# Kernel optimization log

Hardware: AMD Instinct MI355X
Metric: run time of the kernel (lower is better)

## Reference

```python
import jax, jax.numpy as jnp
import numpy as np

# dims (match init_kwargs)
S = 2048      # sequence_length
H = 2048      # hidden_size
NH = 32       # num_attention_heads
KVH = 8       # num_key_value_heads
HD = 64       # head_dim
WIN = 128     # sliding_window
QM = NH // KVH
SM_SCALE = 1.0 / float(np.sqrt(HD))


def _rope_rotate(x, cos, sin):
    # x: [S, n, HD]; cos/sin: [S, HD//2]
    x1, x2 = jnp.split(x, 2, axis=-1)
    c = cos[:, None, :].astype(x.dtype)
    s = sin[:, None, :].astype(x.dtype)
    return jnp.concatenate([x1 * c - x2 * s, x2 * c + x1 * s], axis=-1)


def setup_inputs() -> dict:
    key = jax.random.key(0)
    ks = jax.random.split(key, 6)
    x = jax.random.normal(ks[0], (S, H), jnp.float32)
    qkv_dim = HD * (NH + 2 * KVH)
    qkv_kernel = jax.random.normal(ks[1], (H, qkv_dim), jnp.float32) * 0.02
    qkv_bias = jnp.zeros((qkv_dim,), jnp.float32)
    out_kernel = jax.random.normal(ks[2], (NH * HD, H), jnp.float32) * 0.02
    out_bias = jnp.zeros((H,), jnp.float32)
    sinks = jax.random.normal(ks[3], (NH,), jnp.float32) * 0.02
    # RoPE tables: [S, HD//2]
    pos = np.arange(S, dtype=np.float32)
    inv_freq = 1.0 / (10000.0 ** (np.arange(HD // 2, dtype=np.float32) / (HD // 2)))
    ang = pos[:, None] * inv_freq[None, :]
    cos_table = jnp.asarray(np.cos(ang), jnp.float32)
    sin_table = jnp.asarray(np.sin(ang), jnp.float32)
    # causal + sliding-window additive mask [S, S]
    qi = np.arange(S, dtype=np.int32)[:, None]
    ki = np.arange(S, dtype=np.int32)[None, :]
    m = np.where(ki > qi, -np.inf, 0.0).astype(np.float32)
    m = np.where(ki < qi - WIN, -np.inf, m).astype(np.float32)
    mask = jnp.asarray(m)
    return {"x": x, "qkv_kernel": qkv_kernel, "qkv_bias": qkv_bias,
            "out_kernel": out_kernel, "out_bias": out_bias, "sinks": sinks,
            "cos_table": cos_table, "sin_table": sin_table, "mask": mask}


def reference(x, qkv_kernel, qkv_bias, out_kernel, out_bias, sinks, cos_table, sin_table, mask):
    xf = x.astype(jnp.float32)
    qkv = jnp.dot(xf, qkv_kernel, precision=jax.lax.Precision.HIGHEST) + qkv_bias  # [S, qkv_dim]
    q_end = NH * HD
    k_end = q_end + KVH * HD
    q = qkv[:, :q_end].reshape(S, NH, HD)          # NH = KVH*QM
    k = qkv[:, q_end:k_end].reshape(S, KVH, HD)
    v = qkv[:, k_end:].reshape(S, KVH, HD)
    q = _rope_rotate(q, cos_table, sin_table).reshape(S, KVH, QM, HD)
    k = _rope_rotate(k, cos_table, sin_table)
    # logits: [KVH, QM, S_q, S_k]; K broadcast across q_mult (GQA)
    logits = jnp.einsum('qhmd,khd->hmqk', q, k) * jnp.float32(SM_SCALE)
    logits = logits + mask[None, None, :, :]
    sink = jnp.broadcast_to(sinks.reshape(KVH, QM, 1, 1).astype(jnp.float32), (KVH, QM, S, 1))
    extended = jnp.concatenate([logits, sink], axis=-1)
    weights = jax.nn.softmax(extended, axis=-1)[..., :-1]
    attn = jnp.einsum('hmqk,khd->qhmd', weights, v).reshape(S, NH * HD)
    out = jnp.dot(attn, out_kernel, precision=jax.lax.Precision.HIGHEST) + out_bias
    return out.astype(x.dtype)
```

## Files before the change

### kernel.cpp

```cpp
#include <hip/hip_runtime.h>
#include <hip/hip_bf16.h>
#include <cstdint>

typedef __hip_bfloat16 bf16;
typedef __attribute__((ext_vector_type(8))) __bf16 bf16x8;
typedef __attribute__((ext_vector_type(4))) float f32x4;

static __device__ __forceinline__ void gload_lds16(const void* g, void* l) {
  __builtin_amdgcn_global_load_lds(
      (const __attribute__((address_space(1))) uint32_t*)g,
      (__attribute__((address_space(3))) uint32_t*)l, 16, 0, 0);
}

__global__ void f32_to_bf16_kernel(const float* __restrict__ in, bf16* __restrict__ out, int n4) {
  int i = blockIdx.x * 256 + threadIdx.x;
  if (i >= n4) return;
  const float4 v = reinterpret_cast<const float4*>(in)[i];
  ushort4 o;
  o.x = __builtin_bit_cast(unsigned short, __float2bfloat16(v.x));
  o.y = __builtin_bit_cast(unsigned short, __float2bfloat16(v.y));
  o.z = __builtin_bit_cast(unsigned short, __float2bfloat16(v.z));
  o.w = __builtin_bit_cast(unsigned short, __float2bfloat16(v.w));
  reinterpret_cast<ushort4*>(out)[i] = o;
}

__global__ void transpose_to_bf16_kernel(const float* __restrict__ in, bf16* __restrict__ out,
                                         int R, int C) {
  __shared__ float tile[32][33];
  int c0 = blockIdx.x * 32, r0 = blockIdx.y * 32;
  int tx = threadIdx.x & 31, ty = threadIdx.x >> 5;
#pragma unroll
  for (int i = 0; i < 4; ++i)
    tile[ty + i * 8][tx] = in[(size_t)(r0 + ty + i * 8) * C + c0 + tx];
  __syncthreads();
#pragma unroll
  for (int i = 0; i < 4; ++i)
    out[(size_t)(c0 + ty + i * 8) * R + r0 + tx] = __float2bfloat16(tile[tx][ty + i * 8]);
}

template <int NH, int SSHIFT>
__global__ void rope_kernel(bf16* __restrict__ buf, const float* __restrict__ cosT,
                            const float* __restrict__ sinT) {
  const int idx = blockIdx.x * 256 + threadIdx.x;
  const int c = idx & 3;
  const int h = (idx >> 2) & (NH - 1);
  const int s = idx >> SSHIFT;
  bf16* p = buf + (size_t)s * (NH * 64) + h * 64 + c * 8;
  bf16x8 v1 = *reinterpret_cast<bf16x8*>(p);
  bf16x8 v2 = *reinterpret_cast<bf16x8*>(p + 32);
  const float4 c0 = *reinterpret_cast<const float4*>(&cosT[s * 32 + c * 8]);
  const float4 c1 = *reinterpret_cast<const float4*>(&cosT[s * 32 + c * 8 + 4]);
  const float4 s0 = *reinterpret_cast<const float4*>(&sinT[s * 32 + c * 8]);
  const float4 s1 = *reinterpret_cast<const float4*>(&sinT[s * 32 + c * 8 + 4]);
  const float cs[8] = {c0.x, c0.y, c0.z, c0.w, c1.x, c1.y, c1.z, c1.w};
  const float sn[8] = {s0.x, s0.y, s0.z, s0.w, s1.x, s1.y, s1.z, s1.w};
  bf16x8 o1, o2;
#pragma unroll
  for (int e = 0; e < 8; ++e) {
    const float x1 = (float)v1[e], x2 = (float)v2[e];
    o1[e] = (__bf16)(x1 * cs[e] - x2 * sn[e]);
    o2[e] = (__bf16)(x2 * cs[e] + x1 * sn[e]);
  }
  *reinterpret_cast<bf16x8*>(p) = o1;
  *reinterpret_cast<bf16x8*>(p + 32) = o2;
}

__global__ __launch_bounds__(512, 1)
void gemm1_kernel(const bf16* __restrict__ A, const bf16* __restrict__ Bt,
                  const float* __restrict__ bias,
                  bf16* __restrict__ qb, bf16* __restrict__ kb, bf16* __restrict__ vt) {
  extern __shared__ __align__(16) char smem[];
  constexpr int K = 2048, NK = 32;
  const int lin = blockIdx.x;
  const int wgid = (lin & 7) * 32 + (lin >> 3);
  const int bx = wgid >> 4, by = wgid & 15;
  const int brow = by * 128, bcol = bx * 192;
  const int t = threadIdx.x, lane = t & 63, w = t >> 6;
  const int wr = w >> 2, wc = w & 3;
  const int rr = lane & 15, rg = lane >> 4;

  char* Ab = smem;
  char* Bb = smem + 49152;

  auto stageA = [&](int kt) {
#pragma unroll
    for (int p = 0; p < 2; ++p) {
      const int idx = p * 512 + t;
      const int row = idx >> 3;
      const int cg = (idx & 7) ^ (row & 7);
      gload_lds16(A + (size_t)(brow + row) * K + kt * 64 + cg * 8,
                  Ab + (size_t)(kt % 3) * 16384 + (p * 512 + (t & ~63)) * 16);
    }
  };
  auto stageB = [&](int kt) {
#pragma unroll
    for (int p = 0; p < 3; ++p) {
      const int idx = p * 512 + t;
      const int row = idx >> 3;
      const int cg = (idx & 7) ^ (row & 7);
      gload_lds16(Bt + (size_t)(bcol + row) * K + kt * 64 + cg * 8,
                  Bb + (size_t)(kt % 3) * 24576 + (p * 512 + (t & ~63)) * 16);
    }
  };

  f32x4 acc[4][3];
#pragma unroll
  for (int i = 0; i < 4; ++i)
#pragma unroll
    for (int j = 0; j < 3; ++j) acc[i][j] = f32x4{0.f, 0.f, 0.f, 0.f};

  stageA(0); stageB(0); stageA(1); stageB(1);
  asm volatile("s_waitcnt vmcnt(5)" ::: "memory");
  __builtin_amdgcn_s_barrier();

  for (int kt = 0; kt < NK; ++kt) {
    const char* Ar = Ab + (size_t)(kt % 3) * 16384;
    const char* Br = Bb + (size_t)(kt % 3) * 24576;
#pragma unroll
    for (int ks = 0; ks < 2; ++ks) {
      bf16x8 af[4], bfr[3];
      const int c = ks * 4 + rg;
#pragma unroll
      for (int i = 0; i < 4; ++i) {
        const int row = wr * 64 + i * 16 + rr;
        af[i] = *reinterpret_cast<const bf16x8*>(Ar + row * 128 + ((c ^ (row & 7)) * 16));
      }
#pragma unroll
      for (int j = 0; j < 3; ++j) {
        const int row = wc * 48 + j * 16 + rr;
        bfr[j] = *reinterpret_cast<const bf16x8*>(Br + row * 128 + ((c ^ (row & 7)) * 16));
      }
      if (kt + 2 < NK) {
        if (ks == 0) stageA(kt + 2);
        else         stageB(kt + 2);
      }
      asm volatile("s_waitcnt lgkmcnt(0)" ::: "memory");
      __builtin_amdgcn_sched_barrier(0);
      __builtin_amdgcn_s_setprio(1);
#pragma unroll
      for (int i = 0; i < 4; ++i)
#pragma unroll
        for (int j = 0; j < 3; ++j)
          acc[i][j] = __builtin_amdgcn_mfma_f32_16x16x32_bf16(af[i], bfr[j], acc[i][j], 0, 0, 0);
      __builtin_amdgcn_s_setprio(0);
    }
    if (kt + 2 < NK)      asm volatile("s_waitcnt vmcnt(5)" ::: "memory");
    else if (kt + 1 < NK) asm volatile("s_waitcnt vmcnt(0)" ::: "memory");
    if (kt + 1 < NK) __builtin_amdgcn_s_barrier();
  }

#pragma unroll
  for (int j = 0; j < 3; ++j) {
    const int gcf = bcol + wc * 48 + j * 16;
    const int gc = gcf + rr;
    const float bv = bias[gc];
    if (gcf < 2048) {
#pragma unroll
      for (int i = 0; i < 4; ++i) {
        const int s0 = brow + wr * 64 + i * 16 + rg * 4;
#pragma unroll
        for (int r = 0; r < 4; ++r)
          qb[(size_t)(s0 + r) * 2048 + gc] = __float2bfloat16(acc[i][j][r] + bv);
      }
    } else if (gcf < 2560) {
      const int kc = gc - 2048;
#pragma unroll
      for (int i = 0; i < 4; ++i) {
        const int s0 = brow + wr * 64 + i * 16 + rg * 4;
#pragma unroll
        for (int r = 0; r < 4; ++r)
          kb[(size_t)(s0 + r) * 512 + kc] = __float2bfloat16(acc[i][j][r] + bv);
      }
    } else {
      const int vcol = gc - 2560;
#pragma unroll
      for (int i = 0; i < 4; ++i) {
        ushort4 o;
        o.x = __builtin_bit_cast(unsigned short, __float2bfloat16(acc[i][j][0] + bv));
        o.y = __builtin_bit_cast(unsigned short, __float2bfloat16(acc[i][j][1] + bv));
        o.z = __builtin_bit_cast(unsigned short, __float2bfloat16(acc[i][j][2] + bv));
        o.w = __builtin_bit_cast(unsigned short, __float2bfloat16(acc[i][j][3] + bv));
        *reinterpret_cast<ushort4*>(
            &vt[(size_t)vcol * 2048 + brow + wr * 64 + i * 16 + rg * 4]) = o;
      }
    }
  }
}

__global__ __launch_bounds__(512, 1)
void gemm2_kernel(const bf16* __restrict__ A, const bf16* __restrict__ Bt,
                  const float* __restrict__ bias, float* __restrict__ C) {
  extern __shared__ __align__(16) char smem[];
  constexpr int K = 2048, NK = 32;
  const int lin = blockIdx.x;
  const int wgid = (lin & 7) * 32 + (lin >> 3);
  const int bx = wgid >> 4, by = wgid & 15;
  const int brow = by * 128, bcol = bx * 128;
  const int t = threadIdx.x, lane = t & 63, w = t >> 6;
  const int wr = (w & 3) >> 1, wc = w & 1, khalf = w >> 2;
  const int rr = lane & 15, rg = lane >> 4;

  char* Ab = smem;
  char* Bb = smem + 49152;

  auto stage = [&](int kt) {
#pragma unroll
    for (int p = 0; p < 2; ++p) {
      const int idx = p * 512 + t;
      const int row = idx >> 3;
      const int cg = (idx & 7) ^ (row & 7);
      gload_lds16(A + (size_t)(brow + row) * K + kt * 64 + cg * 8,
                  Ab + (size_t)(kt % 3) * 16384 + (p * 512 + (t & ~63)) * 16);
      gload_lds16(Bt + (size_t)(bcol + row) * K + kt * 64 + cg * 8,
                  Bb + (size_t)(kt % 3) * 16384 + (p * 512 + (t & ~63)) * 16);
    }
  };

  f32x4 acc[4][4];
#pragma unroll
  for (int i = 0; i < 4; ++i)
#pragma unroll
    for (int j = 0; j < 4; ++j) acc[i][j] = f32x4{0.f, 0.f, 0.f, 0.f};

  stage(0); stage(1);
  asm volatile("s_waitcnt vmcnt(4)" ::: "memory");
  __builtin_amdgcn_s_barrier();

  for (int kt = 0; kt < NK; ++kt) {
    const char* Ar = Ab + (size_t)(kt % 3) * 16384;
    const char* Br = Bb + (size_t)(kt % 3) * 16384;
    bf16x8 af[4], bfr[4];
    const int c = khalf * 4 + rg;
#pragma unroll
    for (int i = 0; i < 4; ++i) {
      const int row = wr * 64 + i * 16 + rr;
      af[i] = *reinterpret_cast<const bf16x8*>(Ar + row * 128 + ((c ^ (row & 7)) * 16));
    }
#pragma unroll
    for (int j = 0; j < 4; ++j) {
      const int row = wc * 64 + j * 16 + rr;
      bfr[j] = *reinterpret_cast<const bf16x8*>(Br + row * 128 + ((c ^ (row & 7)) * 16));
    }
    if (kt + 2 < NK) stage(kt + 2);
    asm volatile("s_waitcnt lgkmcnt(0)" ::: "memory");
    __builtin_amdgcn_sched_barrier(0);
    __builtin_amdgcn_s_setprio(1);
#pragma unroll
    for (int i = 0; i < 4; ++i)
#pragma unroll
      for (int j = 0; j < 4; ++j)
        acc[i][j] = __builtin_amdgcn_mfma_f32_16x16x32_bf16(af[i], bfr[j], acc[i][j], 0, 0, 0);
    __builtin_amdgcn_s_setprio(0);
    if (kt + 2 < NK)      asm volatile("s_waitcnt vmcnt(4)" ::: "memory");
    else if (kt + 1 < NK) asm volatile("s_waitcnt vmcnt(0)" ::: "memory");
    if (kt + 1 < NK) __builtin_amdgcn_s_barrier();
  }

  __syncthreads();
  float* red = (float*)smem;
  if (w >= 4) {
#pragma unroll
    for (int i = 0; i < 4; ++i)
#pragma unroll
      for (int j = 0; j < 4; ++j)
        *reinterpret_cast<f32x4*>(&red[(w - 4) * 4096 + (i * 4 + j) * 256 + lane * 4]) = acc[i][j];
  }
  __syncthreads();
  if (w < 4) {
#pragma unroll
    for (int i = 0; i < 4; ++i)
#pragma unroll
      for (int j = 0; j < 4; ++j) {
        const f32x4 o = *reinterpret_cast<const f32x4*>(&red[w * 4096 + (i * 4 + j) * 256 + lane * 4]);
        const int gc = bcol + wc * 64 + j * 16 + rr;
        const float bv = bias[gc];
        const int r0 = brow + wr * 64 + i * 16 + rg * 4;
#pragma unroll
        for (int r = 0; r < 4; ++r)
          C[(size_t)(r0 + r) * 2048 + gc] = acc[i][j][r] + o[r] + bv;
      }
  }
}

__global__ __launch_bounds__(256, 2)
void attn_kernel(const bf16* __restrict__ Q, const bf16* __restrict__ Kb,
                 const bf16* __restrict__ Vt, const float* __restrict__ sinks,
                 bf16* __restrict__ aout) {
  extern __shared__ __align__(16) char smem[];
  const int hk = blockIdx.x;
  const int q0 = blockIdx.y * 32;
  const int k0 = q0 - 128;
  const int t = threadIdx.x, w = t >> 6, lane = t & 63;
  const int cl = lane & 15, rg = lane >> 4;
  const int head = hk * 4 + w;

  char* Ks = smem;
  char* Ps = smem + 20480 + w * 12288;

#pragma unroll
  for (int p = 0; p < 5; ++p) {
    const int idx = p * 256 + t;
    const int row = idx >> 3, c = idx & 7;
    int key = k0 + row;
    if (key < 0) key = 0;
    gload_lds16(Kb + (size_t)key * 512 + hk * 64 + ((c ^ (row & 7)) << 3),
                Ks + (size_t)(p * 256 + (t & ~63)) * 16);
  }
  __syncthreads();

  bf16x8 aq[2][2];
#pragma unroll
  for (int qf = 0; qf < 2; ++qf)
#pragma unroll
    for (int ks = 0; ks < 2; ++ks)
      aq[qf][ks] = *reinterpret_cast<const bf16x8*>(
          Q + (size_t)(q0 + qf * 16 + cl) * 2048 + head * 64 + ks * 32 + rg * 8);

  f32x4 acc[2][10];
#pragma unroll
  for (int qf = 0; qf < 2; ++qf)
#pragma unroll
    for (int nf = 0; nf < 10; ++nf) acc[qf][nf] = f32x4{0.f, 0.f, 0.f, 0.f};

#pragma unroll
  for (int nf = 0; nf < 10; ++nf) {
    const int row = nf * 16 + cl;
    bf16x8 bk[2];
#pragma unroll
    for (int ks = 0; ks < 2; ++ks) {
      const int chunk = ks * 4 + rg;
      bk[ks] = *reinterpret_cast<const bf16x8*>(
          Ks + row * 128 + ((chunk ^ (row & 7)) << 4));
    }
#pragma unroll
    for (int qf = 0; qf < 2; ++qf)
#pragma unroll
      for (int ks = 0; ks < 2; ++ks)
        acc[qf][nf] = __builtin_amdgcn_mfma_f32_16x16x32_bf16(aq[qf][ks], bk[ks], acc[qf][nf], 0, 0, 0);
  }

  const float sinkv = sinks[head];
  const float scale = 0.125f;
  const int cfloor = 128 - q0;
#pragma unroll
  for (int qf = 0; qf < 2; ++qf)
#pragma unroll
    for (int r = 0; r < 4; ++r) {
      const int rowb = qf * 16 + rg * 4 + r;
      int cmin = rowb;
      if (cfloor > cmin) cmin = cfloor;
      const int cmax = rowb + 128;
      float m = sinkv;
      float pv[10];
#pragma unroll
      for (int nf = 0; nf < 10; ++nf) {
        const int cc = nf * 16 + cl;
        float lv = (cc >= cmin && cc <= cmax) ? acc[qf][nf][r] * scale : -INFINITY;
        pv[nf] = lv;
        m = fmaxf(m, lv);
      }
#pragma unroll
      for (int off = 1; off < 16; off <<= 1)
        m = fmaxf(m, __shfl_xor(m, off, 64));
      float sum = 0.f;
#pragma unroll
      for (int nf = 0; nf < 10; ++nf) {
        const float p = __expf(pv[nf] - m);
        pv[nf] = p;
        sum += p;
      }
#pragma unroll
      for (int off = 1; off < 16; off <<= 1)
        sum += __shfl_xor(sum, off, 64);
      sum += __expf(sinkv - m);
      const float inv = 1.f / sum;
#pragma unroll
      for (int nf = 0; nf < 10; ++nf) {
        const int col = nf * 16 + cl;
        const int chunk = col >> 3;
        *reinterpret_cast<bf16*>(Ps + rowb * 384 + ((chunk ^ (rowb & 7)) << 4) + (cl & 7) * 2) =
            __float2bfloat16(pv[nf] * inv);
      }
    }

  asm volatile("s_waitcnt lgkmcnt(0)" ::: "memory");
  __builtin_amdgcn_sched_barrier(0);

  f32x4 oacc[2][4];
#pragma unroll
  for (int qf = 0; qf < 2; ++qf)
#pragma unroll
    for (int j = 0; j < 4; ++j) oacc[qf][j] = f32x4{0.f, 0.f, 0.f, 0.f};

#pragma unroll
  for (int ks = 0; ks < 5; ++ks) {
    bf16x8 pa[2];
#pragma unroll
    for (int qf = 0; qf < 2; ++qf) {
      const int row = qf * 16 + cl;
      const int chunk = ks * 4 + rg;
      pa[qf] = *reinterpret_cast<const bf16x8*>(
          Ps + row * 384 + ((chunk ^ (row & 7)) << 4));
    }
    int key = k0 + ks * 32 + rg * 8;
    if (key < 0) key = 0;
#pragma unroll
    for (int j = 0; j < 4; ++j) {
      const bf16x8 bv = *reinterpret_cast<const bf16x8*>(
          Vt + ((size_t)hk * 64 + j * 16 + cl) * 2048 + key);
#pragma unroll
      for (int qf = 0; qf < 2; ++qf)
        oacc[qf][j] = __builtin_amdgcn_mfma_f32_16x16x32_bf16(pa[qf], bv, oacc[qf][j], 0, 0, 0);
    }
  }

#pragma unroll
  for (int qf = 0; qf < 2; ++qf)
#pragma unroll
    for (int j = 0; j < 4; ++j)
#pragma unroll
      for (int r = 0; r < 4; ++r) {
        const int gr = q0 + qf * 16 + rg * 4 + r;
        const int gc = head * 64 + j * 16 + cl;
        aout[(size_t)gr * 2048 + gc] = __float2bfloat16(oacc[qf][j][r]);
      }
}

extern "C" void kernel_launch(void* const* d_in, const int* in_sizes, int n_in,
                              void* d_out, int out_size, void* d_ws, size_t ws_size,
                              hipStream_t stream) {
  const float* x     = (const float*)d_in[0];
  const float* w1    = (const float*)d_in[1];
  const float* b1    = (const float*)d_in[2];
  const float* w2    = (const float*)d_in[3];
  const float* b2    = (const float*)d_in[4];
  const float* sinks = (const float*)d_in[5];
  const float* cosT  = (const float*)d_in[6];
  const float* sinT  = (const float*)d_in[7];
  float* out = (float*)d_out;

  char* ws = (char*)d_ws;
  bf16* xb   = (bf16*)(ws);
  bf16* w1t  = (bf16*)(ws + 8388608);
  bf16* w2t  = (bf16*)(ws + 20971520);
  bf16* qbuf = (bf16*)(ws + 29360128);
  bf16* kbuf = (bf16*)(ws + 37748736);
  bf16* vt   = (bf16*)(ws + 39845888);
  bf16* attn = (bf16*)(ws + 41943040);
  (void)in_sizes; (void)n_in; (void)out_size; (void)ws_size;

  f32_to_bf16_kernel<<<4096, 256, 0, stream>>>(x, xb, 1048576);
  transpose_to_bf16_kernel<<<dim3(96, 64), 256, 0, stream>>>(w1, w1t, 2048, 3072);
  transpose_to_bf16_kernel<<<dim3(64, 64), 256, 0, stream>>>(w2, w2t, 2048, 2048);
  gemm1_kernel<<<256, 512, 122880, stream>>>(xb, w1t, b1, qbuf, kbuf, vt);
  rope_kernel<32, 7><<<1024, 256, 0, stream>>>(qbuf, cosT, sinT);
  rope_kernel<8, 5><<<256, 256, 0, stream>>>(kbuf, cosT, sinT);
  attn_kernel<<<dim3(8, 64), 256, 69632, stream>>>(qbuf, kbuf, vt, sinks, attn);
  gemm2_kernel<<<256, 512, 98304, stream>>>(attn, w2t, b2, out);
}
```

Before: 92.96 us.

## Fuse prep kernels, fold Q RoPE into attention, halve attention query tile

Merges the x conversion and both weight transposes into a single launch, which removes two kernel launches. Q RoPE is now applied in registers inside the attention kernel, so the separate Q rope pass over the Q buffer is dropped. The attention block now covers 16 query rows instead of 32, with 144 keys plus a zero-padded P tile, smaller LDS use and three blocks per CU. The cost is less reuse of each loaded K/V tile per block and twice as many attention blocks.

```diff
diff --git a/kernel.cpp b/kernel.cpp
--- a/kernel.cpp
+++ b/kernel.cpp
@@ -12,23 +12,36 @@
       (__attribute__((address_space(3))) uint32_t*)l, 16, 0, 0);
 }
 
-__global__ void f32_to_bf16_kernel(const float* __restrict__ in, bf16* __restrict__ out, int n4) {
-  int i = blockIdx.x * 256 + threadIdx.x;
-  if (i >= n4) return;
-  const float4 v = reinterpret_cast<const float4*>(in)[i];
-  ushort4 o;
-  o.x = __builtin_bit_cast(unsigned short, __float2bfloat16(v.x));
-  o.y = __builtin_bit_cast(unsigned short, __float2bfloat16(v.y));
-  o.z = __builtin_bit_cast(unsigned short, __float2bfloat16(v.z));
-  o.w = __builtin_bit_cast(unsigned short, __float2bfloat16(v.w));
-  reinterpret_cast<ushort4*>(out)[i] = o;
-}
-
-__global__ void transpose_to_bf16_kernel(const float* __restrict__ in, bf16* __restrict__ out,
-                                         int R, int C) {
+__global__ __launch_bounds__(256)
+void prep_kernel(const float* __restrict__ x, const float* __restrict__ w1,
+                 const float* __restrict__ w2, bf16* __restrict__ xb,
+                 bf16* __restrict__ w1t, bf16* __restrict__ w2t) {
   __shared__ float tile[32][33];
-  int c0 = blockIdx.x * 32, r0 = blockIdx.y * 32;
-  int tx = threadIdx.x & 31, ty = threadIdx.x >> 5;
+  const int lin = blockIdx.x;
+  const int t = threadIdx.x;
+  if (lin < 4096) {
+    const int i = lin * 256 + t;
+    const float4 v = reinterpret_cast<const float4*>(x)[i];
+    ushort4 o;
+    o.x = __builtin_bit_cast(unsigned short, __float2bfloat16(v.x));
+    o.y = __builtin_bit_cast(unsigned short, __float2bfloat16(v.y));
+    o.z = __builtin_bit_cast(unsigned short, __float2bfloat16(v.z));
+    o.w = __builtin_bit_cast(unsigned short, __float2bfloat16(v.w));
+    reinterpret_cast<ushort4*>(xb)[i] = o;
+    return;
+  }
+  const float* in;
+  bf16* out;
+  int R, C, bx, by;
+  if (lin < 10240) {
+    const int tl = lin - 4096;
+    in = w1; out = w1t; R = 2048; C = 3072; bx = tl % 96; by = tl / 96;
+  } else {
+    const int tl = lin - 10240;
+    in = w2; out = w2t; R = 2048; C = 2048; bx = tl & 63; by = tl >> 6;
+  }
+  const int c0 = bx * 32, r0 = by * 32;
+  const int tx = t & 31, ty = t >> 5;
 #pragma unroll
   for (int i = 0; i < 4; ++i)
     tile[ty + i * 8][tx] = in[(size_t)(r0 + ty + i * 8) * C + c0 + tx];
@@ -282,23 +295,24 @@
   }
 }
 
-__global__ __launch_bounds__(256, 2)
+__global__ __launch_bounds__(256, 3)
 void attn_kernel(const bf16* __restrict__ Q, const bf16* __restrict__ Kb,
                  const bf16* __restrict__ Vt, const float* __restrict__ sinks,
+                 const float* __restrict__ cosT, const float* __restrict__ sinT,
                  bf16* __restrict__ aout) {
   extern __shared__ __align__(16) char smem[];
   const int hk = blockIdx.x;
-  const int q0 = blockIdx.y * 32;
+  const int q0 = blockIdx.y * 16;
   const int k0 = q0 - 128;
   const int t = threadIdx.x, w = t >> 6, lane = t & 63;
   const int cl = lane & 15, rg = lane >> 4;
   const int head = hk * 4 + w;
 
   char* Ks = smem;
-  char* Ps = smem + 20480 + w * 12288;
-
-#pragma unroll
-  for (int p = 0; p < 5; ++p) {
+  char* Ps = smem + 18432 + w * 6144;
+
+#pragma unroll
+  for (int p = 0; p < 4; ++p) {
     const int idx = p * 256 + t;
     const int row = idx >> 3, c = idx & 7;
     int key = k0 + row;
@@ -306,124 +320,126 @@
     gload_lds16(Kb + (size_t)key * 512 + hk * 64 + ((c ^ (row & 7)) << 3),
                 Ks + (size_t)(p * 256 + (t & ~63)) * 16);
   }
+  if (t < 128) {
+    const int idx = 1024 + t;
+    const int row = idx >> 3, c = idx & 7;
+    gload_lds16(Kb + (size_t)(k0 + row) * 512 + hk * 64 + ((c ^ (row & 7)) << 3),
+                Ks + (size_t)(1024 + (t & ~63)) * 16);
+  }
+
+  const int qrow = q0 + cl;
+  bf16x8 aq[2];
+  {
+    const bf16* qp = Q + (size_t)qrow * 2048 + head * 64 + rg * 8;
+    const bf16x8 q1 = *reinterpret_cast<const bf16x8*>(qp);
+    const bf16x8 q2 = *reinterpret_cast<const bf16x8*>(qp + 32);
+    const float4 c0 = *reinterpret_cast<const float4*>(&cosT[qrow * 32 + rg * 8]);
+    const float4 c1 = *reinterpret_cast<const float4*>(&cosT[qrow * 32 + rg * 8 + 4]);
+    const float4 s0 = *reinterpret_cast<const float4*>(&sinT[qrow * 32 + rg * 8]);
+    const float4 s1 = *reinterpret_cast<const float4*>(&sinT[qrow * 32 + rg * 8 + 4]);
+    const float cs[8] = {c0.x, c0.y, c0.z, c0.w, c1.x, c1.y, c1.z, c1.w};
+    const float sn[8] = {s0.x, s0.y, s0.z, s0.w, s1.x, s1.y, s1.z, s1.w};
+#pragma unroll
+    for (int e = 0; e < 8; ++e) {
+      const float x1 = (float)q1[e], x2 = (float)q2[e];
+      aq[0][e] = (__bf16)(x1 * cs[e] - x2 * sn[e]);
+      aq[1][e] = (__bf16)(x2 * cs[e] + x1 * sn[e]);
+    }
+  }
   __syncthreads();
 
-  bf16x8 aq[2][2];
-#pragma unroll
-  for (int qf = 0; qf < 2; ++qf)
-#pragma unroll
-    for (int ks = 0; ks < 2; ++ks)
-      aq[qf][ks] = *reinterpret_cast<const bf16x8*>(
-          Q + (size_t)(q0 + qf * 16 + cl) * 2048 + head * 64 + ks * 32 + rg * 8);
-
-  f32x4 acc[2][10];
-#pragma unroll
-  for (int qf = 0; qf < 2; ++qf)
-#pragma unroll
-    for (int nf = 0; nf < 10; ++nf) acc[qf][nf] = f32x4{0.f, 0.f, 0.f, 0.f};
-
-#pragma unroll
-  for (int nf = 0; nf < 10; ++nf) {
+  f32x4 acc[9];
+#pragma unroll
+  for (int nf = 0; nf < 9; ++nf) acc[nf] = f32x4{0.f, 0.f, 0.f, 0.f};
+#pragma unroll
+  for (int nf = 0; nf < 9; ++nf) {
     const int row = nf * 16 + cl;
-    bf16x8 bk[2];
 #pragma unroll
     for (int ks = 0; ks < 2; ++ks) {
       const int chunk = ks * 4 + rg;
-      bk[ks] = *reinterpret_cast<const bf16x8*>(
+      const bf16x8 bk = *reinterpret_cast<const bf16x8*>(
           Ks + row * 128 + ((chunk ^ (row & 7)) << 4));
-    }
-#pragma unroll
-    for (int qf = 0; qf < 2; ++qf)
-#pragma unroll
-      for (int ks = 0; ks < 2; ++ks)
-        acc[qf][nf] = __builtin_amdgcn_mfma_f32_16x16x32_bf16(aq[qf][ks], bk[ks], acc[qf][nf], 0, 0, 0);
+      acc[nf] = __builtin_amdgcn_mfma_f32_16x16x32_bf16(aq[ks], bk, acc[nf], 0, 0, 0);
+    }
   }
 
   const float sinkv = sinks[head];
   const float scale = 0.125f;
   const int cfloor = 128 - q0;
 #pragma unroll
-  for (int qf = 0; qf < 2; ++qf)
-#pragma unroll
-    for (int r = 0; r < 4; ++r) {
-      const int rowb = qf * 16 + rg * 4 + r;
-      int cmin = rowb;
-      if (cfloor > cmin) cmin = cfloor;
-      const int cmax = rowb + 128;
-      float m = sinkv;
-      float pv[10];
-#pragma unroll
-      for (int nf = 0; nf < 10; ++nf) {
-        const int cc = nf * 16 + cl;
-        float lv = (cc >= cmin && cc <= cmax) ? acc[qf][nf][r] * scale : -INFINITY;
-        pv[nf] = lv;
-        m = fmaxf(m, lv);
-      }
-#pragma unroll
-      for (int off = 1; off < 16; off <<= 1)
-        m = fmaxf(m, __shfl_xor(m, off, 64));
-      float sum = 0.f;
-#pragma unroll
-      for (int nf = 0; nf < 10; ++nf) {
-        const float p = __expf(pv[nf] - m);
-        pv[nf] = p;
-        sum += p;
-      }
-#pragma unroll
-      for (int off = 1; off < 16; off <<= 1)
-        sum += __shfl_xor(sum, off, 64);
-      sum += __expf(sinkv - m);
-      const float inv = 1.f / sum;
-#pragma unroll
-      for (int nf = 0; nf < 10; ++nf) {
-        const int col = nf * 16 + cl;
-        const int chunk = col >> 3;
-        *reinterpret_cast<bf16*>(Ps + rowb * 384 + ((chunk ^ (rowb & 7)) << 4) + (cl & 7) * 2) =
-            __float2bfloat16(pv[nf] * inv);
-      }
-    }
+  for (int r = 0; r < 4; ++r) {
+    const int rowb = rg * 4 + r;
+    int cmin = rowb;
+    if (cfloor > cmin) cmin = cfloor;
+    const int cmax = rowb + 128;
+    float m = sinkv;
+    float pv[9];
+#pragma unroll
+    for (int nf = 0; nf < 9; ++nf) {
+      const int cc = nf * 16 + cl;
+      float lv = (cc >= cmin && cc <= cmax) ? acc[nf][r] * scale : -INFINITY;
+      pv[nf] = lv;
+      m = fmaxf(m, lv);
+    }
+#pragma unroll
+    for (int off = 1; off < 16; off <<= 1)
+      m = fmaxf(m, __shfl_xor(m, off, 64));
+    float sum = 0.f;
+#pragma unroll
+    for (int nf = 0; nf < 9; ++nf) {
+      const float p = __expf(pv[nf] - m);
+      pv[nf] = p;
+      sum += p;
+    }
+#pragma unroll
+    for (int off = 1; off < 16; off <<= 1)
+      sum += __shfl_xor(sum, off, 64);
+    sum += __expf(sinkv - m);
+    const float inv = 1.f / sum;
+#pragma unroll
+    for (int nf = 0; nf < 9; ++nf) {
+      const int col = nf * 16 + cl;
+      const int chunk = col >> 3;
+      *reinterpret_cast<bf16*>(Ps + rowb * 384 + ((chunk ^ (rowb & 7)) << 4) + (cl & 7) * 2) =
+          __float2bfloat16(pv[nf] * inv);
+    }
+    {
+      const int col = 144 + cl;
+      const int chunk = col >> 3;
+      *reinterpret_cast<bf16*>(Ps + rowb * 384 + ((chunk ^ (rowb & 7)) << 4) + (cl & 7) * 2) =
+          __float2bfloat16(0.f);
+    }
+  }
 
   asm volatile("s_waitcnt lgkmcnt(0)" ::: "memory");
   __builtin_amdgcn_sched_barrier(0);
 
-  f32x4 oacc[2][4];
-#pragma unroll
-  for (int qf = 0; qf < 2; ++qf)
-#pragma unroll
-    for (int j = 0; j < 4; ++j) oacc[qf][j] = f32x4{0.f, 0.f, 0.f, 0.f};
-
+  f32x4 oacc[4];
+#pragma unroll
+  for (int j = 0; j < 4; ++j) oacc[j] = f32x4{0.f, 0.f, 0.f, 0.f};
 #pragma unroll
   for (int ks = 0; ks < 5; ++ks) {
-    bf16x8 pa[2];
-#pragma unroll
-    for (int qf = 0; qf < 2; ++qf) {
-      const int row = qf * 16 + cl;
-      const int chunk = ks * 4 + rg;
-      pa[qf] = *reinterpret_cast<const bf16x8*>(
-          Ps + row * 384 + ((chunk ^ (row & 7)) << 4));
-    }
+    const int chunk = ks * 4 + rg;
+    const bf16x8 pa = *reinterpret_cast<const bf16x8*>(
+        Ps + cl * 384 + ((chunk ^ (cl & 7)) << 4));
     int key = k0 + ks * 32 + rg * 8;
     if (key < 0) key = 0;
 #pragma unroll
     for (int j = 0; j < 4; ++j) {
       const bf16x8 bv = *reinterpret_cast<const bf16x8*>(
           Vt + ((size_t)hk * 64 + j * 16 + cl) * 2048 + key);
-#pragma unroll
-      for (int qf = 0; qf < 2; ++qf)
-        oacc[qf][j] = __builtin_amdgcn_mfma_f32_16x16x32_bf16(pa[qf], bv, oacc[qf][j], 0, 0, 0);
-    }
-  }
-
-#pragma unroll
-  for (int qf = 0; qf < 2; ++qf)
-#pragma unroll
-    for (int j = 0; j < 4; ++j)
-#pragma unroll
-      for (int r = 0; r < 4; ++r) {
-        const int gr = q0 + qf * 16 + rg * 4 + r;
-        const int gc = head * 64 + j * 16 + cl;
-        aout[(size_t)gr * 2048 + gc] = __float2bfloat16(oacc[qf][j][r]);
-      }
+      oacc[j] = __builtin_amdgcn_mfma_f32_16x16x32_bf16(pa, bv, oacc[j], 0, 0, 0);
+    }
+  }
+
+#pragma unroll
+  for (int j = 0; j < 4; ++j)
+#pragma unroll
+    for (int r = 0; r < 4; ++r) {
+      const int gr = q0 + rg * 4 + r;
+      const int gc = head * 64 + j * 16 + cl;
+      aout[(size_t)gr * 2048 + gc] = __float2bfloat16(oacc[j][r]);
+    }
 }
 
 extern "C" void kernel_launch(void* const* d_in, const int* in_sizes, int n_in,
@@ -449,12 +465,9 @@
   bf16* attn = (bf16*)(ws + 41943040);
   (void)in_sizes; (void)n_in; (void)out_size; (void)ws_size;
 
-  f32_to_bf16_kernel<<<4096, 256, 0, stream>>>(x, xb, 1048576);
-  transpose_to_bf16_kernel<<<dim3(96, 64), 256, 0, stream>>>(w1, w1t, 2048, 3072);
-  transpose_to_bf16_kernel<<<dim3(64, 64), 256, 0, stream>>>(w2, w2t, 2048, 2048);
+  prep_kernel<<<14336, 256, 0, stream>>>(x, w1, w2, xb, w1t, w2t);
   gemm1_kernel<<<256, 512, 122880, stream>>>(xb, w1t, b1, qbuf, kbuf, vt);
-  rope_kernel<32, 7><<<1024, 256, 0, stream>>>(qbuf, cosT, sinT);
   rope_kernel<8, 5><<<256, 256, 0, stream>>>(kbuf, cosT, sinT);
-  attn_kernel<<<dim3(8, 64), 256, 69632, stream>>>(qbuf, kbuf, vt, sinks, attn);
+  attn_kernel<<<dim3(8, 128), 256, 43008, stream>>>(qbuf, kbuf, vt, sinks, cosT, sinT, attn);
   gemm2_kernel<<<256, 512, 98304, stream>>>(attn, w2t, b2, out);
 }
```

Result: no change. 93.78 us (+0.9%).

## Merge input conversion kernels and fuse Q RoPE into attention kernel

Applied to the files above, without the earlier changes.

Folds the x cast and the two weight transpose/cast kernels into one prep launch that dispatches on block index. The separate Q RoPE kernel is dropped: the attention kernel now applies the rotation to Q in registers as it loads Q, reading the cos/sin tables directly. This removes two launches and one full read-modify-write pass over the Q buffer. In exchange the attention kernel does extra loads and arithmetic on its critical path, and the Q load now overlaps the K tile prefetch before the barrier.

```diff
diff --git a/kernel.cpp b/kernel.cpp
--- a/kernel.cpp
+++ b/kernel.cpp
@@ -12,23 +12,36 @@
       (__attribute__((address_space(3))) uint32_t*)l, 16, 0, 0);
 }
 
-__global__ void f32_to_bf16_kernel(const float* __restrict__ in, bf16* __restrict__ out, int n4) {
-  int i = blockIdx.x * 256 + threadIdx.x;
-  if (i >= n4) return;
-  const float4 v = reinterpret_cast<const float4*>(in)[i];
-  ushort4 o;
-  o.x = __builtin_bit_cast(unsigned short, __float2bfloat16(v.x));
-  o.y = __builtin_bit_cast(unsigned short, __float2bfloat16(v.y));
-  o.z = __builtin_bit_cast(unsigned short, __float2bfloat16(v.z));
-  o.w = __builtin_bit_cast(unsigned short, __float2bfloat16(v.w));
-  reinterpret_cast<ushort4*>(out)[i] = o;
-}
-
-__global__ void transpose_to_bf16_kernel(const float* __restrict__ in, bf16* __restrict__ out,
-                                         int R, int C) {
+__global__ __launch_bounds__(256)
+void prep_kernel(const float* __restrict__ x, const float* __restrict__ w1,
+                 const float* __restrict__ w2, bf16* __restrict__ xb,
+                 bf16* __restrict__ w1t, bf16* __restrict__ w2t) {
   __shared__ float tile[32][33];
-  int c0 = blockIdx.x * 32, r0 = blockIdx.y * 32;
-  int tx = threadIdx.x & 31, ty = threadIdx.x >> 5;
+  const int lin = blockIdx.x;
+  const int t = threadIdx.x;
+  if (lin < 4096) {
+    const int i = lin * 256 + t;
+    const float4 v = reinterpret_cast<const float4*>(x)[i];
+    ushort4 o;
+    o.x = __builtin_bit_cast(unsigned short, __float2bfloat16(v.x));
+    o.y = __builtin_bit_cast(unsigned short, __float2bfloat16(v.y));
+    o.z = __builtin_bit_cast(unsigned short, __float2bfloat16(v.z));
+    o.w = __builtin_bit_cast(unsigned short, __float2bfloat16(v.w));
+    reinterpret_cast<ushort4*>(xb)[i] = o;
+    return;
+  }
+  const float* in;
+  bf16* out;
+  int R, C, bx, by;
+  if (lin < 10240) {
+    const int tl = lin - 4096;
+    in = w1; out = w1t; R = 2048; C = 3072; bx = tl % 96; by = tl / 96;
+  } else {
+    const int tl = lin - 10240;
+    in = w2; out = w2t; R = 2048; C = 2048; bx = tl & 63; by = tl >> 6;
+  }
+  const int c0 = bx * 32, r0 = by * 32;
+  const int tx = t & 31, ty = t >> 5;
 #pragma unroll
   for (int i = 0; i < 4; ++i)
     tile[ty + i * 8][tx] = in[(size_t)(r0 + ty + i * 8) * C + c0 + tx];
@@ -285,6 +298,7 @@
 __global__ __launch_bounds__(256, 2)
 void attn_kernel(const bf16* __restrict__ Q, const bf16* __restrict__ Kb,
                  const bf16* __restrict__ Vt, const float* __restrict__ sinks,
+                 const float* __restrict__ cosT, const float* __restrict__ sinT,
                  bf16* __restrict__ aout) {
   extern __shared__ __align__(16) char smem[];
   const int hk = blockIdx.x;
@@ -306,15 +320,28 @@
     gload_lds16(Kb + (size_t)key * 512 + hk * 64 + ((c ^ (row & 7)) << 3),
                 Ks + (size_t)(p * 256 + (t & ~63)) * 16);
   }
+
+  bf16x8 aq[2][2];
+#pragma unroll
+  for (int qf = 0; qf < 2; ++qf) {
+    const int qrow = q0 + qf * 16 + cl;
+    const bf16* qp = Q + (size_t)qrow * 2048 + head * 64 + rg * 8;
+    const bf16x8 q1 = *reinterpret_cast<const bf16x8*>(qp);
+    const bf16x8 q2 = *reinterpret_cast<const bf16x8*>(qp + 32);
+    const float4 c0 = *reinterpret_cast<const float4*>(&cosT[qrow * 32 + rg * 8]);
+    const float4 c1 = *reinterpret_cast<const float4*>(&cosT[qrow * 32 + rg * 8 + 4]);
+    const float4 s0 = *reinterpret_cast<const float4*>(&sinT[qrow * 32 + rg * 8]);
+    const float4 s1 = *reinterpret_cast<const float4*>(&sinT[qrow * 32 + rg * 8 + 4]);
+    const float cs[8] = {c0.x, c0.y, c0.z, c0.w, c1.x, c1.y, c1.z, c1.w};
+    const float sn[8] = {s0.x, s0.y, s0.z, s0.w, s1.x, s1.y, s1.z, s1.w};
+#pragma unroll
+    for (int e = 0; e < 8; ++e) {
+      const float x1 = (float)q1[e], x2 = (float)q2[e];
+      aq[qf][0][e] = (__bf16)(x1 * cs[e] - x2 * sn[e]);
+      aq[qf][1][e] = (__bf16)(x2 * cs[e] + x1 * sn[e]);
+    }
+  }
   __syncthreads();
-
-  bf16x8 aq[2][2];
-#pragma unroll
-  for (int qf = 0; qf < 2; ++qf)
-#pragma unroll
-    for (int ks = 0; ks < 2; ++ks)
-      aq[qf][ks] = *reinterpret_cast<const bf16x8*>(
-          Q + (size_t)(q0 + qf * 16 + cl) * 2048 + head * 64 + ks * 32 + rg * 8);
 
   f32x4 acc[2][10];
 #pragma unroll
@@ -449,12 +476,9 @@
   bf16* attn = (bf16*)(ws + 41943040);
   (void)in_sizes; (void)n_in; (void)out_size; (void)ws_size;
 
-  f32_to_bf16_kernel<<<4096, 256, 0, stream>>>(x, xb, 1048576);
-  transpose_to_bf16_kernel<<<dim3(96, 64), 256, 0, stream>>>(w1, w1t, 2048, 3072);
-  transpose_to_bf16_kernel<<<dim3(64, 64), 256, 0, stream>>>(w2, w2t, 2048, 2048);
+  prep_kernel<<<14336, 256, 0, stream>>>(x, w1, w2, xb, w1t, w2t);
   gemm1_kernel<<<256, 512, 122880, stream>>>(xb, w1t, b1, qbuf, kbuf, vt);
-  rope_kernel<32, 7><<<1024, 256, 0, stream>>>(qbuf, cosT, sinT);
   rope_kernel<8, 5><<<256, 256, 0, stream>>>(kbuf, cosT, sinT);
-  attn_kernel<<<dim3(8, 64), 256, 69632, stream>>>(qbuf, kbuf, vt, sinks, attn);
+  attn_kernel<<<dim3(8, 64), 256, 69632, stream>>>(qbuf, kbuf, vt, sinks, cosT, sinT, attn);
   gemm2_kernel<<<256, 512, 98304, stream>>>(attn, w2t, b2, out);
 }
```

Result: faster. 86.72 us (-6.7%).
